# Kernel optimization log

Hardware: AMD Instinct MI355X
Metric: run time of the kernel (lower is better)

Reference implementation:

```python
import jax, jax.numpy as jnp
import numpy as np
from jax import lax

VOCAB, EMB, HID, MAXD, NCLS = 50000, 512, 512, 1024, 20
S, B = 512, 64

def setup_inputs() -> dict:
    key = jax.random.key(0)
    ks = jax.random.split(key, 16)
    sc = 0.05
    return {
        "inp": jax.random.randint(ks[0], (S, B), 0, VOCAB),
        "emb_table": jax.random.normal(ks[1], (VOCAB, EMB), jnp.float32) * sc,
        "c_l0": jax.random.normal(ks[2], (HID,), jnp.float32) * sc,
        "c_r0": jax.random.normal(ks[3], (HID,), jnp.float32) * sc,
        "W_l": jax.random.normal(ks[4], (HID, HID), jnp.float32) * sc,
        "b_l": jnp.zeros((HID,), jnp.float32),
        "W_r": jax.random.normal(ks[5], (HID, HID), jnp.float32) * sc,
        "b_r": jnp.zeros((HID,), jnp.float32),
        "W_sl": jax.random.normal(ks[6], (HID, EMB), jnp.float32) * sc,
        "b_sl": jnp.zeros((HID,), jnp.float32),
        "W_sr": jax.random.normal(ks[7], (EMB, HID), jnp.float32) * sc,  # emb_dim==hid_dim required by source
        "b_sr": jnp.zeros((EMB,), jnp.float32),
        "W_max": jax.random.normal(ks[8], (MAXD, 2 * HID + EMB), jnp.float32) * sc,
        "b_max": jnp.zeros((MAXD,), jnp.float32),
        "W_doc": jax.random.normal(ks[9], (NCLS, MAXD), jnp.float32) * sc,
        "b_doc": jnp.zeros((NCLS,), jnp.float32),
    }

def reference(inp, emb_table, c_l0, c_r0, W_l, b_l, W_r, b_r,
              W_sl, b_sl, W_sr, b_sr, W_max, b_max, W_doc, b_doc):
    # inp: [S, B] int; emb: [S, B, E]
    emb = emb_table[inp]
    # precomputed per-token projections (done once, outside the recurrence)
    emb_ls = jnp.einsum('sbe,he->sbh', emb, W_sl) + b_sl  # [S,B,H]
    emb_rs = jnp.einsum('sbe,he->sbh', emb, W_sr) + b_sr  # [S,B,H]

    def step(W, b):
        def f(c, e):  # c: [B,H], e: [B,H]
            c = jnp.tanh(c @ W.T + b + e)
            return c, c
        return f

    batch = inp.shape[1]
    c_l_init = jnp.broadcast_to(c_l0, (batch, HID))
    c_r_init = jnp.broadcast_to(c_r0, (batch, HID))
    _, c_ls = lax.scan(step(W_l, b_l), c_l_init, emb_ls)          # [S,B,H] left-to-right
    _, c_rs_rev = lax.scan(step(W_r, b_r), c_r_init, emb_rs[::-1])  # scanned right-to-left
    c_rs = c_rs_rev[::-1]                                          # re-aligned to positions

    cat = jnp.concatenate([c_ls, emb, c_rs], axis=2)               # [S,B,2H+E]
    y = jnp.tanh(jnp.einsum('sbc,mc->sbm', cat, W_max) + b_max)    # [S,B,M]
    y_max = jnp.max(y, axis=0)                                     # [B,M] max-pool over seq
    logits = y_max @ W_doc.T + b_doc                               # [B,C]
    return jax.nn.log_softmax(logits, axis=-1)
```

## Files before the change

kernel.cpp:

```cpp
#include <hip/hip_runtime.h>
#include <hip/hip_bf16.h>
#include <cstdint>
#include <cstddef>

#define SS   512
#define BB   64
#define EMBD 512
#define HIDD 512
#define MAXD 1024
#define NCLS 20
#define KCAT 1536
#define ROWS (SS*BB)

__device__ __forceinline__ uint16_t f2bf(float f) {
  uint32_t u = __float_as_uint(f);
  uint32_t r = u + 0x7fffu + ((u >> 16) & 1u);
  return (uint16_t)(r >> 16);
}
__device__ __forceinline__ float bf2f(uint32_t h) {
  return __uint_as_float(h << 16);
}
__device__ __forceinline__ uint32_t pk2(float a, float b) {
  return (uint32_t)f2bf(a) | ((uint32_t)f2bf(b) << 16);
}

__device__ __forceinline__ float fast_tanh(float x) {
  float ax = __builtin_fabsf(x);
  float e  = __builtin_amdgcn_exp2f(ax * -2.885390081777927f);
  float r  = (1.f - e) * __builtin_amdgcn_rcpf(1.f + e);
  return __builtin_copysignf(r, x);
}

#if defined(__has_builtin)
#if __has_builtin(__builtin_amdgcn_fdot2_f32_bf16)
#define USE_BF16_DOT2 1
#endif
#endif

#ifdef USE_BF16_DOT2
typedef __bf16 bf16x2_t __attribute__((ext_vector_type(2)));
__device__ __forceinline__ float dot2bf(uint32_t w, uint32_t c, float acc) {
  return __builtin_amdgcn_fdot2_f32_bf16(__builtin_bit_cast(bf16x2_t, w),
                                         __builtin_bit_cast(bf16x2_t, c), acc, false);
}
#else
__device__ __forceinline__ float dot2bf(uint32_t w, uint32_t c, float acc) {
  float w0 = __uint_as_float(w << 16);
  float w1 = __uint_as_float(w & 0xffff0000u);
  float c0 = __uint_as_float(c << 16);
  float c1 = __uint_as_float(c & 0xffff0000u);
  return fmaf(w1, c1, fmaf(w0, c0, acc));
}
#endif

__device__ __forceinline__ void gl_lds16(const void* g, void* l) {
  __builtin_amdgcn_global_load_lds((const __attribute__((address_space(1))) void*)g,
                                   (__attribute__((address_space(3))) void*)l,
                                   16, 0, 0);
}

typedef short v8s __attribute__((ext_vector_type(8)));
typedef float v4f __attribute__((ext_vector_type(4)));

__global__ __launch_bounds__(256) void prep_kernel(
    const int* __restrict__ inp, const float* __restrict__ table,
    const float* __restrict__ Wsl, const float* __restrict__ Wsr,
    const float* __restrict__ Wl,  const float* __restrict__ Wr,
    const float* __restrict__ Wmax,
    uint16_t* __restrict__ cat, uint16_t* __restrict__ wslb,
    uint16_t* __restrict__ wsrb, uint16_t* __restrict__ wlb,
    uint16_t* __restrict__ wrb, uint16_t* __restrict__ wmaxb)
{
  const int blk = blockIdx.x, t = threadIdx.x;
  if (blk < 8192) {
    const int r = blk * 4 + (t >> 6);
    const int lane = t & 63;
    const int token = inp[r];
    const float4* src = (const float4*)(table + (size_t)token * EMBD);
    uint16_t* dst = cat + (size_t)r * KCAT + 512;
#pragma unroll
    for (int p = 0; p < 2; ++p) {
      const int slot = lane + 64 * p;
      float4 v = src[slot];
      uint2 o;
      o.x = pk2(v.x, v.y);
      o.y = pk2(v.z, v.w);
      *(uint2*)(dst + slot * 4) = o;
    }
  } else {
    size_t flat = (size_t)(blk - 8192) * 2048 + (size_t)t * 8;
    const float* src; uint16_t* dst; size_t off;
    if (flat < 262144)       { src = Wsl;  dst = wslb;  off = flat; }
    else if (flat < 524288)  { src = Wsr;  dst = wsrb;  off = flat - 262144; }
    else if (flat < 786432)  { src = Wl;   dst = wlb;   off = flat - 524288; }
    else if (flat < 1048576) { src = Wr;   dst = wrb;   off = flat - 786432; }
    else                     { src = Wmax; dst = wmaxb; off = flat - 1048576; }
    float4 v0 = *(const float4*)(src + off);
    float4 v1 = *(const float4*)(src + off + 4);
    uint4 o;
    o.x = pk2(v0.x, v0.y); o.y = pk2(v0.z, v0.w);
    o.z = pk2(v1.x, v1.y); o.w = pk2(v1.z, v1.w);
    *(uint4*)(dst + off) = o;
  }
}

template<int MODE>
__global__ __launch_bounds__(256, 2) void gemm_kernel(
    const uint16_t* __restrict__ A, int lda, int K,
    const uint16_t* __restrict__ W0, const uint16_t* __restrict__ W1,
    const float* __restrict__ bias0, const float* __restrict__ bias1,
    uint16_t* __restrict__ outb, float* __restrict__ partial)
{
  __shared__ unsigned char smem[32768];
  uint16_t* lA = (uint16_t*)smem;
  uint16_t* lW = (uint16_t*)(smem + 16384);

  const int tid = threadIdx.x;
  const int mb = blockIdx.x, nb = blockIdx.y;
  const int m0 = mb * 128, n0 = nb * 128;

  const uint16_t* Wp = W0;
  const float* biasp = bias0;
  int nr0 = n0;
  if (MODE == 0 && n0 >= 512) { Wp = W1; biasp = bias1; nr0 = n0 - 512; }

  const int w = tid >> 6, lane = tid & 63;
  const int mw = w & 1, nw = w >> 1;

  v4f acc[4][4];
#pragma unroll
  for (int i = 0; i < 4; ++i)
#pragma unroll
    for (int j = 0; j < 4; ++j) {
      v4f z = {0.f, 0.f, 0.f, 0.f};
      acc[i][j] = z;
    }

  const int r_st = tid >> 3;
  const int u_st = tid & 7;

  for (int kk = 0; kk < K; kk += 64) {
    __syncthreads();
#pragma unroll
    for (int p = 0; p < 4; ++p) {
      const int r = p * 32 + r_st;
      gl_lds16(A + (size_t)(m0 + r) * lda + kk + u_st * 8, lA + (p * 256 + tid) * 8);
    }
#pragma unroll
    for (int p = 0; p < 4; ++p) {
      const int r = p * 32 + r_st;
      gl_lds16(Wp + (size_t)(nr0 + r) * K + kk + u_st * 8, lW + (p * 256 + tid) * 8);
    }
    __syncthreads();
#pragma unroll
    for (int ks = 0; ks < 2; ++ks) {
      v8s af[4], wf[4];
#pragma unroll
      for (int i = 0; i < 4; ++i)
        af[i] = *(const v8s*)&lA[(mw * 64 + i * 16 + (lane & 15)) * 64 + ks * 32 + (lane >> 4) * 8];
#pragma unroll
      for (int j = 0; j < 4; ++j)
        wf[j] = *(const v8s*)&lW[(nw * 64 + j * 16 + (lane & 15)) * 64 + ks * 32 + (lane >> 4) * 8];
#pragma unroll
      for (int i = 0; i < 4; ++i)
#pragma unroll
        for (int j = 0; j < 4; ++j)
          acc[i][j] = __builtin_amdgcn_mfma_f32_16x16x32_bf16(af[i], wf[j], acc[i][j], 0, 0, 0);
    }
  }

  __syncthreads();

  if (MODE == 0) {
#pragma unroll
    for (int i = 0; i < 4; ++i)
#pragma unroll
      for (int j = 0; j < 4; ++j) {
        const int nl = nw * 64 + j * 16 + (lane & 15);
        const float bv = biasp[nr0 + nl];
        const int colg = n0 + nl;
#pragma unroll
        for (int r = 0; r < 4; ++r) {
          const int rowg = m0 + mw * 64 + i * 16 + (lane >> 4) * 4 + r;
          outb[(size_t)rowg * 1024 + colg] = f2bf(acc[i][j][r] + bv);
        }
      }
  } else {
    float* lred = (float*)smem;
    if (mw == 1) {
#pragma unroll
      for (int i = 0; i < 4; ++i)
#pragma unroll
        for (int j = 0; j < 4; ++j) {
          const int nl = nw * 64 + j * 16 + (lane & 15);
          const float bv = biasp[nr0 + nl];
#pragma unroll
          for (int r = 0; r < 4; ++r) {
            const int bl = i * 16 + (lane >> 4) * 4 + r;
            lred[bl * 128 + nl] = fast_tanh(acc[i][j][r] + bv);
          }
        }
    }
    __syncthreads();
    if (mw == 0) {
#pragma unroll
      for (int i = 0; i < 4; ++i)
#pragma unroll
        for (int j = 0; j < 4; ++j) {
          const int nl = nw * 64 + j * 16 + (lane & 15);
          const float bv = biasp[nr0 + nl];
#pragma unroll
          for (int r = 0; r < 4; ++r) {
            const int bl = i * 16 + (lane >> 4) * 4 + r;
            const float v = fast_tanh(acc[i][j][r] + bv);
            partial[((size_t)mb * 64 + bl) * 1024 + n0 + nl] = fmaxf(v, lred[bl * 128 + nl]);
          }
        }
    }
  }
}

__global__ __launch_bounds__(512, 1) void scan_kernel(
    const uint16_t* __restrict__ ee,
    const uint16_t* __restrict__ wlb, const uint16_t* __restrict__ wrb,
    const float* __restrict__ bl, const float* __restrict__ br,
    const float* __restrict__ cl0, const float* __restrict__ cr0,
    uint16_t* __restrict__ cat,
    uint64_t* __restrict__ cbuf)
{
  const int tid = threadIdx.x;
  const int bid = blockIdx.x;
  const int b    = bid & 63;
  const int d    = (bid >> 6) & 1;
  const int half = bid >> 7;
  const int lane = tid & 63;

  const int hp = tid & 127;
  const int kq = tid >> 7;
  const bool remote = (kq >> 1) != half;

  __shared__ __align__(16) uint32_t cfull[256];
  __shared__ float2 part2[4 * 128];

  uint32_t wAa[64], wBa[64];
  {
    const uint16_t* wsrc = (d ? wrb : wlb) + (size_t)(half * 256 + 2 * hp) * HIDD + kq * 128;
    const uint4* pA = (const uint4*)wsrc;
    const uint4* pB = (const uint4*)(wsrc + HIDD);
#pragma unroll
    for (int j = 0; j < 16; ++j) {
      uint4 qa = pA[j], qb = pB[j];
      wAa[4 * j] = qa.x; wAa[4 * j + 1] = qa.y; wAa[4 * j + 2] = qa.z; wAa[4 * j + 3] = qa.w;
      wBa[4 * j] = qb.x; wBa[4 * j + 1] = qb.y; wBa[4 * j + 2] = qb.z; wBa[4 * j + 3] = qb.w;
    }
  }
  if (tid < 256) {
    const float* c0v = d ? cr0 : cl0;
    float2 cv0 = ((const float2*)c0v)[tid];
    cfull[tid] = pk2(cv0.x, cv0.y);
  }

  const int fbase = half * 256;
  const unsigned ft = (unsigned)(tid - fbase);
  const int fp = tid - fbase;

  float2 biasv = {0.f, 0.f};
  if (ft < 128u) {
    const float* bvec = d ? br : bl;
    biasv = ((const float2*)bvec)[half * 128 + fp];
  }
  __syncthreads();

  const size_t ecol = (size_t)(d * 512 + half * 256 + 2 * fp);
  const int fcol = (d ? 1024 : 0) + half * 256 + 2 * fp;

  const int pslot = ((kq & 1) << 6) | lane;
  const int pbid  = bid ^ 128;

  uint32_t ep0 = 0, ep1 = 0;
  if (ft < 128u) {
    const int s0i = d ? 511 : 0;
    const int s1i = d ? 510 : 1;
    ep0 = *(const uint32_t*)&ee[(size_t)(s0i * BB + b) * 1024 + ecol];
    ep1 = *(const uint32_t*)&ee[(size_t)(s1i * BB + b) * 1024 + ecol];
  }

  uint32_t prPrev = 0;
  int sPrev = -1;

  for (int i = 0; i < 512; ++i) {
    const int s = d ? (511 - i) : i;
    uint32_t ep2 = 0;
    if (ft < 128u) {
      const int i2 = (i + 2) & 511;
      const int s2 = d ? (511 - i2) : i2;
      ep2 = *(const uint32_t*)&ee[(size_t)(s2 * BB + b) * 1024 + ecol];
      if (sPrev >= 0)
        *(uint32_t*)&cat[(size_t)(sPrev * BB + b) * KCAT + fcol] = prPrev;
    }

    uint32_t cv;
    if (remote && i != 0) {
      const uint64_t want = (uint64_t)(uint32_t)i;
      const uint64_t* slot = &cbuf[(size_t)(((((i & 1) ^ 1)) * 256 + pbid) * 128 + pslot)];
      uint64_t v = __hip_atomic_load(slot, __ATOMIC_RELAXED, __HIP_MEMORY_SCOPE_AGENT);
      while ((v >> 32) != want) {
        __builtin_amdgcn_s_sleep(1);
        v = __hip_atomic_load(slot, __ATOMIC_RELAXED, __HIP_MEMORY_SCOPE_AGENT);
      }
      cv = (uint32_t)v;
    } else {
      cv = cfull[kq * 64 + lane];
    }

    {
      float a0 = 0.f, a1 = 0.f, a2 = 0.f, a3 = 0.f;
#pragma unroll
      for (int j = 0; j < 32; ++j) {
        const uint32_t cj0 = __builtin_amdgcn_readlane(cv, 2 * j);
        const uint32_t cj1 = __builtin_amdgcn_readlane(cv, 2 * j + 1);
        a0 = dot2bf(wAa[2 * j],     cj0, a0);
        a2 = dot2bf(wBa[2 * j],     cj0, a2);
        a1 = dot2bf(wAa[2 * j + 1], cj1, a1);
        a3 = dot2bf(wBa[2 * j + 1], cj1, a3);
      }
      float2 pv; pv.x = a0 + a1; pv.y = a2 + a3;
      part2[kq * 128 + hp] = pv;
    }

    __syncthreads();

    if (ft < 128u) {
      float2 q0 = part2[fp];
      float2 q1 = part2[128 + fp];
      float2 q2 = part2[256 + fp];
      float2 q3 = part2[384 + fp];
      float s0 = ((q0.x + q1.x) + (q2.x + q3.x)) + biasv.x + bf2f(ep0 & 0xffffu);
      float s1 = ((q0.y + q1.y) + (q2.y + q3.y)) + biasv.y + bf2f(ep0 >> 16);
      uint32_t pr = pk2(fast_tanh(s0), fast_tanh(s1));
      if (i != 511) {
        uint64_t pkt = ((uint64_t)(uint32_t)(i + 1) << 32) | (uint64_t)pr;
        __hip_atomic_store(&cbuf[(size_t)(((i & 1) * 256 + bid) * 128 + fp)],
                           pkt, __ATOMIC_RELAXED, __HIP_MEMORY_SCOPE_AGENT);
        cfull[half * 128 + fp] = pr;
        prPrev = pr; sPrev = s;
      } else {
        *(uint32_t*)&cat[(size_t)(s * BB + b) * KCAT + fcol] = pr;
      }
    }

    if (i == 511) break;
    __syncthreads();

    ep0 = ep1; ep1 = ep2;
  }
}

__global__ __launch_bounds__(256) void final_kernel(
    const float* __restrict__ partial, const float* __restrict__ Wdoc,
    const float* __restrict__ bdoc, float* __restrict__ out)
{
  const int b = blockIdx.x, t = threadIdx.x;
  __shared__ float ym[1024];
  __shared__ float lg[32];
  float m0 = -2.f, m1 = -2.f, m2 = -2.f, m3 = -2.f;
  for (int mg = 0; mg < 256; ++mg) {
    const float* p = partial + ((size_t)mg * 64 + b) * 1024;
    m0 = fmaxf(m0, p[t]);
    m1 = fmaxf(m1, p[t + 256]);
    m2 = fmaxf(m2, p[t + 512]);
    m3 = fmaxf(m3, p[t + 768]);
  }
  ym[t] = m0; ym[t + 256] = m1; ym[t + 512] = m2; ym[t + 768] = m3;
  __syncthreads();
  if (t < NCLS) {
    const float* wr = Wdoc + (size_t)t * 1024;
    float a0 = 0.f, a1 = 0.f, a2 = 0.f, a3 = 0.f;
    for (int n = 0; n < 1024; n += 4) {
      a0 = fmaf(ym[n], wr[n], a0);
      a1 = fmaf(ym[n + 1], wr[n + 1], a1);
      a2 = fmaf(ym[n + 2], wr[n + 2], a2);
      a3 = fmaf(ym[n + 3], wr[n + 3], a3);
    }
    lg[t] = (a0 + a1) + (a2 + a3) + bdoc[t];
  }
  __syncthreads();
  if (t < NCLS) {
    float mx = -1e30f;
    for (int c = 0; c < NCLS; ++c) mx = fmaxf(mx, lg[c]);
    float ssum = 0.f;
    for (int c = 0; c < NCLS; ++c) ssum += expf(lg[c] - mx);
    out[b * NCLS + t] = lg[t] - mx - logf(ssum);
  }
}

extern "C" void kernel_launch(void* const* d_in, const int* in_sizes, int n_in,
                              void* d_out, int out_size, void* d_ws, size_t ws_size,
                              hipStream_t stream) {
  const int*   inp   = (const int*)  d_in[0];
  const float* table = (const float*)d_in[1];
  const float* cl0   = (const float*)d_in[2];
  const float* cr0   = (const float*)d_in[3];
  const float* Wl    = (const float*)d_in[4];
  const float* bl    = (const float*)d_in[5];
  const float* Wr    = (const float*)d_in[6];
  const float* br    = (const float*)d_in[7];
  const float* Wsl   = (const float*)d_in[8];
  const float* bsl   = (const float*)d_in[9];
  const float* Wsr   = (const float*)d_in[10];
  const float* bsr   = (const float*)d_in[11];
  const float* Wmax  = (const float*)d_in[12];
  const float* bmax  = (const float*)d_in[13];
  const float* Wdoc  = (const float*)d_in[14];
  const float* bdoc  = (const float*)d_in[15];

  uint8_t* ws = (uint8_t*)d_ws;
  uint16_t* cat     = (uint16_t*)(ws);
  uint16_t* ee      = (uint16_t*)(ws + 100663296);
  float*    partial = (float*)   (ws + 167772160);
  uint16_t* wslb    = (uint16_t*)(ws + 234881024);
  uint16_t* wsrb    = (uint16_t*)(ws + 235405312);
  uint16_t* wmaxb   = (uint16_t*)(ws + 235929600);
  uint16_t* wlb     = (uint16_t*)(ws + 239075328);
  uint16_t* wrb     = (uint16_t*)(ws + 239599616);
  uint64_t* cbuf    = (uint64_t*)(ws + 167772160);

  prep_kernel<<<9472, 256, 0, stream>>>(inp, table, Wsl, Wsr, Wl, Wr, Wmax,
                                        cat, wslb, wsrb, wlb, wrb, wmaxb);
  gemm_kernel<0><<<dim3(256, 8), 256, 0, stream>>>(cat + 512, KCAT, 512, wslb, wsrb,
                                                   bsl, bsr, ee, nullptr);
  scan_kernel<<<256, 512, 0, stream>>>(ee, wlb, wrb, bl, br, cl0, cr0, cat, cbuf);
  gemm_kernel<1><<<dim3(256, 8), 256, 0, stream>>>(cat, KCAT, KCAT, wmaxb, nullptr,
                                                   bmax, nullptr, nullptr, partial);
  final_kernel<<<64, 256, 0, stream>>>(partial, Wdoc, bdoc, (float*)d_out);
}
```

Before: 1.028 ms.

## Batch scan recurrence over 16 sequences per block using MFMA bf16

```diff
diff --git a/kernel.cpp b/kernel.cpp
--- a/kernel.cpp
+++ b/kernel.cpp
@@ -30,28 +30,6 @@
   float r  = (1.f - e) * __builtin_amdgcn_rcpf(1.f + e);
   return __builtin_copysignf(r, x);
 }
-
-#if defined(__has_builtin)
-#if __has_builtin(__builtin_amdgcn_fdot2_f32_bf16)
-#define USE_BF16_DOT2 1
-#endif
-#endif
-
-#ifdef USE_BF16_DOT2
-typedef __bf16 bf16x2_t __attribute__((ext_vector_type(2)));
-__device__ __forceinline__ float dot2bf(uint32_t w, uint32_t c, float acc) {
-  return __builtin_amdgcn_fdot2_f32_bf16(__builtin_bit_cast(bf16x2_t, w),
-                                         __builtin_bit_cast(bf16x2_t, c), acc, false);
-}
-#else
-__device__ __forceinline__ float dot2bf(uint32_t w, uint32_t c, float acc) {
-  float w0 = __uint_as_float(w << 16);
-  float w1 = __uint_as_float(w & 0xffff0000u);
-  float c0 = __uint_as_float(c << 16);
-  float c1 = __uint_as_float(c & 0xffff0000u);
-  return fmaf(w1, c1, fmaf(w0, c0, acc));
-}
-#endif
 
 __device__ __forceinline__ void gl_lds16(const void* g, void* l) {
   __builtin_amdgcn_global_load_lds((const __attribute__((address_space(1))) void*)g,
@@ -230,130 +208,161 @@
 {
   const int tid = threadIdx.x;
   const int bid = blockIdx.x;
-  const int b    = bid & 63;
-  const int d    = (bid >> 6) & 1;
-  const int half = bid >> 7;
+  const int half = bid >> 3;
+  const int g    = (bid >> 1) & 3;
+  const int d    = bid & 1;
+  const int bg   = g * 16;
+  const int pbid = bid ^ 8;
+
+  const int w    = tid >> 6;
   const int lane = tid & 63;
-
-  const int hp = tid & 127;
-  const int kq = tid >> 7;
-  const bool remote = (kq >> 1) != half;
-
-  __shared__ __align__(16) uint32_t cfull[256];
-  __shared__ float2 part2[4 * 128];
-
-  uint32_t wAa[64], wBa[64];
+  const int m4   = (lane >> 4) * 4;
+  const int ncol = lane & 15;
+  const int h0   = half * 256 + w * 32 + ncol;
+  const int h1   = h0 + 16;
+  const int ph0  = (1 - half) * 256 + w * 32 + ncol;
+  const int ph1  = ph0 + 16;
+
+  __shared__ __align__(16) uint16_t Abuf[2][8192];
+
+#define SWZ(batch, chunk) ((((batch) * 64) + ((chunk) ^ ((batch) & 7))) * 16)
+
+  const uint16_t* wsrc = d ? wrb : wlb;
+
+  v8s wf0[16], wf1[16];
   {
-    const uint16_t* wsrc = (d ? wrb : wlb) + (size_t)(half * 256 + 2 * hp) * HIDD + kq * 128;
-    const uint4* pA = (const uint4*)wsrc;
-    const uint4* pB = (const uint4*)(wsrc + HIDD);
-#pragma unroll
-    for (int j = 0; j < 16; ++j) {
-      uint4 qa = pA[j], qb = pB[j];
-      wAa[4 * j] = qa.x; wAa[4 * j + 1] = qa.y; wAa[4 * j + 2] = qa.z; wAa[4 * j + 3] = qa.w;
-      wBa[4 * j] = qb.x; wBa[4 * j + 1] = qb.y; wBa[4 * j + 2] = qb.z; wBa[4 * j + 3] = qb.w;
-    }
-  }
-  if (tid < 256) {
+    const uint16_t* p0 = wsrc + (size_t)h0 * 512 + (lane >> 4) * 8;
+    const uint16_t* p1 = wsrc + (size_t)h1 * 512 + (lane >> 4) * 8;
+#pragma unroll
+    for (int kt = 0; kt < 16; ++kt) {
+      wf0[kt] = *(const v8s*)(p0 + kt * 32);
+      wf1[kt] = *(const v8s*)(p1 + kt * 32);
+    }
+  }
+
+  {
     const float* c0v = d ? cr0 : cl0;
-    float2 cv0 = ((const float2*)c0v)[tid];
-    cfull[tid] = pk2(cv0.x, cv0.y);
-  }
-
-  const int fbase = half * 256;
-  const unsigned ft = (unsigned)(tid - fbase);
-  const int fp = tid - fbase;
-
-  float2 biasv = {0.f, 0.f};
-  if (ft < 128u) {
-    const float* bvec = d ? br : bl;
-    biasv = ((const float2*)bvec)[half * 128 + fp];
-  }
+    const int batch = tid >> 5;
+#pragma unroll
+    for (int cc = 0; cc < 2; ++cc) {
+      const int chunk = (tid & 31) * 2 + cc;
+      const float* src = c0v + chunk * 8;
+      uint4 o;
+      o.x = pk2(src[0], src[1]); o.y = pk2(src[2], src[3]);
+      o.z = pk2(src[4], src[5]); o.w = pk2(src[6], src[7]);
+      *(uint4*)((char*)Abuf[0] + SWZ(batch, chunk)) = o;
+    }
+  }
+
+  const float* bvec = d ? br : bl;
+  const float bias0v = bvec[h0];
+  const float bias1v = bvec[h1];
+
+  const int ec0 = d * 512 + h0, ec1 = d * 512 + h1;
+  uint32_t erA[8], erB[8];
+  {
+    const int s0 = d ? 511 : 0, s1 = d ? 510 : 1;
+#pragma unroll
+    for (int r = 0; r < 4; ++r) {
+      erA[r]     = *(const uint16_t*)&ee[(size_t)(s0 * 64 + bg + m4 + r) * 1024 + ec0];
+      erA[4 + r] = *(const uint16_t*)&ee[(size_t)(s0 * 64 + bg + m4 + r) * 1024 + ec1];
+      erB[r]     = *(const uint16_t*)&ee[(size_t)(s1 * 64 + bg + m4 + r) * 1024 + ec0];
+      erB[4 + r] = *(const uint16_t*)&ee[(size_t)(s1 * 64 + bg + m4 + r) * 1024 + ec1];
+    }
+  }
+
+  const int catbase = (d ? 1024 : 0) + half * 256;
+  const int rbBatch = tid >> 5, rbCl = tid & 31;
+  const int rbChunk = half * 32 + rbCl;
+
   __syncthreads();
 
-  const size_t ecol = (size_t)(d * 512 + half * 256 + 2 * fp);
-  const int fcol = (d ? 1024 : 0) + half * 256 + 2 * fp;
-
-  const int pslot = ((kq & 1) << 6) | lane;
-  const int pbid  = bid ^ 128;
-
-  uint32_t ep0 = 0, ep1 = 0;
-  if (ft < 128u) {
-    const int s0i = d ? 511 : 0;
-    const int s1i = d ? 510 : 1;
-    ep0 = *(const uint32_t*)&ee[(size_t)(s0i * BB + b) * 1024 + ecol];
-    ep1 = *(const uint32_t*)&ee[(size_t)(s1i * BB + b) * 1024 + ecol];
-  }
-
-  uint32_t prPrev = 0;
-  int sPrev = -1;
-
-  for (int i = 0; i < 512; ++i) {
-    const int s = d ? (511 - i) : i;
-    uint32_t ep2 = 0;
-    if (ft < 128u) {
-      const int i2 = (i + 2) & 511;
-      const int s2 = d ? (511 - i2) : i2;
-      ep2 = *(const uint32_t*)&ee[(size_t)(s2 * BB + b) * 1024 + ecol];
-      if (sPrev >= 0)
-        *(uint32_t*)&cat[(size_t)(sPrev * BB + b) * KCAT + fcol] = prPrev;
-    }
-
-    uint32_t cv;
-    if (remote && i != 0) {
-      const uint64_t want = (uint64_t)(uint32_t)i;
-      const uint64_t* slot = &cbuf[(size_t)(((((i & 1) ^ 1)) * 256 + pbid) * 128 + pslot)];
-      uint64_t v = __hip_atomic_load(slot, __ATOMIC_RELAXED, __HIP_MEMORY_SCOPE_AGENT);
-      while ((v >> 32) != want) {
-        __builtin_amdgcn_s_sleep(1);
-        v = __hip_atomic_load(slot, __ATOMIC_RELAXED, __HIP_MEMORY_SCOPE_AGENT);
-      }
-      cv = (uint32_t)v;
+  auto step = [&](int i, uint32_t (&er)[8]) {
+    if (i > 0) {
+      const int sP = d ? (512 - i) : (i - 1);
+      uint4 v = *(const uint4*)((char*)Abuf[i & 1] + SWZ(rbBatch, rbChunk));
+      *(uint4*)&cat[(size_t)(sP * 64 + bg + rbBatch) * KCAT + catbase + rbCl * 8] = v;
+    }
+
+    v4f a00 = {0.f, 0.f, 0.f, 0.f}, a01 = {0.f, 0.f, 0.f, 0.f};
+    v4f a10 = {0.f, 0.f, 0.f, 0.f}, a11 = {0.f, 0.f, 0.f, 0.f};
+#pragma unroll
+    for (int kt = 0; kt < 16; ++kt) {
+      v8s af = *(const v8s*)((char*)Abuf[i & 1] + SWZ(lane & 15, kt * 4 + (lane >> 4)));
+      if (kt & 1) {
+        a01 = __builtin_amdgcn_mfma_f32_16x16x32_bf16(af, wf0[kt], a01, 0, 0, 0);
+        a11 = __builtin_amdgcn_mfma_f32_16x16x32_bf16(af, wf1[kt], a11, 0, 0, 0);
+      } else {
+        a00 = __builtin_amdgcn_mfma_f32_16x16x32_bf16(af, wf0[kt], a00, 0, 0, 0);
+        a10 = __builtin_amdgcn_mfma_f32_16x16x32_bf16(af, wf1[kt], a10, 0, 0, 0);
+      }
+    }
+
+    float v0[4], v1[4];
+#pragma unroll
+    for (int r = 0; r < 4; ++r) {
+      v0[r] = fast_tanh(a00[r] + a01[r] + bias0v + bf2f(er[r]));
+      v1[r] = fast_tanh(a10[r] + a11[r] + bias1v + bf2f(er[4 + r]));
+    }
+
+    if (i < 510) {
+      const int s2 = d ? (509 - i) : (i + 2);
+#pragma unroll
+      for (int r = 0; r < 4; ++r) {
+        er[r]     = *(const uint16_t*)&ee[(size_t)(s2 * 64 + bg + m4 + r) * 1024 + ec0];
+        er[4 + r] = *(const uint16_t*)&ee[(size_t)(s2 * 64 + bg + m4 + r) * 1024 + ec1];
+      }
+    }
+
+    char* An = (char*)Abuf[(i + 1) & 1];
+    if (i != 511) {
+      const uint64_t want = (uint64_t)(uint32_t)(i + 1);
+#pragma unroll
+      for (int r = 0; r < 4; ++r) {
+        uint64_t pkt = (want << 32) | (uint64_t)pk2(v0[r], v1[r]);
+        __hip_atomic_store(&cbuf[(size_t)(((i & 1) * 16 + bid) * 2048 + tid * 4 + r)],
+                           pkt, __ATOMIC_RELAXED, __HIP_MEMORY_SCOPE_AGENT);
+      }
+#pragma unroll
+      for (int r = 0; r < 4; ++r) {
+        *(uint16_t*)(An + SWZ(m4 + r, h0 >> 3) + (h0 & 7) * 2) = f2bf(v0[r]);
+        *(uint16_t*)(An + SWZ(m4 + r, h1 >> 3) + (h1 & 7) * 2) = f2bf(v1[r]);
+      }
+      __builtin_amdgcn_sched_barrier(0);
+#pragma unroll
+      for (int r = 0; r < 4; ++r) {
+        const uint64_t* slot =
+            &cbuf[(size_t)(((i & 1) * 16 + pbid) * 2048 + tid * 4 + r)];
+        uint64_t v = __hip_atomic_load(slot, __ATOMIC_RELAXED, __HIP_MEMORY_SCOPE_AGENT);
+        while ((v >> 32) != want) {
+          __builtin_amdgcn_s_sleep(1);
+          v = __hip_atomic_load(slot, __ATOMIC_RELAXED, __HIP_MEMORY_SCOPE_AGENT);
+        }
+        *(uint16_t*)(An + SWZ(m4 + r, ph0 >> 3) + (ph0 & 7) * 2) = (uint16_t)(v & 0xffffu);
+        *(uint16_t*)(An + SWZ(m4 + r, ph1 >> 3) + (ph1 & 7) * 2) = (uint16_t)((v >> 16) & 0xffffu);
+      }
+      __syncthreads();
     } else {
-      cv = cfull[kq * 64 + lane];
-    }
-
-    {
-      float a0 = 0.f, a1 = 0.f, a2 = 0.f, a3 = 0.f;
-#pragma unroll
-      for (int j = 0; j < 32; ++j) {
-        const uint32_t cj0 = __builtin_amdgcn_readlane(cv, 2 * j);
-        const uint32_t cj1 = __builtin_amdgcn_readlane(cv, 2 * j + 1);
-        a0 = dot2bf(wAa[2 * j],     cj0, a0);
-        a2 = dot2bf(wBa[2 * j],     cj0, a2);
-        a1 = dot2bf(wAa[2 * j + 1], cj1, a1);
-        a3 = dot2bf(wBa[2 * j + 1], cj1, a3);
-      }
-      float2 pv; pv.x = a0 + a1; pv.y = a2 + a3;
-      part2[kq * 128 + hp] = pv;
-    }
-
-    __syncthreads();
-
-    if (ft < 128u) {
-      float2 q0 = part2[fp];
-      float2 q1 = part2[128 + fp];
-      float2 q2 = part2[256 + fp];
-      float2 q3 = part2[384 + fp];
-      float s0 = ((q0.x + q1.x) + (q2.x + q3.x)) + biasv.x + bf2f(ep0 & 0xffffu);
-      float s1 = ((q0.y + q1.y) + (q2.y + q3.y)) + biasv.y + bf2f(ep0 >> 16);
-      uint32_t pr = pk2(fast_tanh(s0), fast_tanh(s1));
-      if (i != 511) {
-        uint64_t pkt = ((uint64_t)(uint32_t)(i + 1) << 32) | (uint64_t)pr;
-        __hip_atomic_store(&cbuf[(size_t)(((i & 1) * 256 + bid) * 128 + fp)],
-                           pkt, __ATOMIC_RELAXED, __HIP_MEMORY_SCOPE_AGENT);
-        cfull[half * 128 + fp] = pr;
-        prPrev = pr; sPrev = s;
-      } else {
-        *(uint32_t*)&cat[(size_t)(s * BB + b) * KCAT + fcol] = pr;
-      }
-    }
-
-    if (i == 511) break;
-    __syncthreads();
-
-    ep0 = ep1; ep1 = ep2;
-  }
+#pragma unroll
+      for (int r = 0; r < 4; ++r) {
+        *(uint16_t*)(An + SWZ(m4 + r, h0 >> 3) + (h0 & 7) * 2) = f2bf(v0[r]);
+        *(uint16_t*)(An + SWZ(m4 + r, h1 >> 3) + (h1 & 7) * 2) = f2bf(v1[r]);
+      }
+    }
+  };
+
+  for (int ii = 0; ii < 256; ++ii) {
+    step(2 * ii, erA);
+    step(2 * ii + 1, erB);
+  }
+
+  __syncthreads();
+  {
+    const int sL = d ? 0 : 511;
+    uint4 v = *(const uint4*)((char*)Abuf[0] + SWZ(rbBatch, rbChunk));
+    *(uint4*)&cat[(size_t)(sL * 64 + bg + rbBatch) * KCAT + catbase + rbCl * 8] = v;
+  }
+#undef SWZ
 }
 
 __global__ __launch_bounds__(256) void final_kernel(
@@ -429,7 +438,7 @@
                                         cat, wslb, wsrb, wlb, wrb, wmaxb);
   gemm_kernel<0><<<dim3(256, 8), 256, 0, stream>>>(cat + 512, KCAT, 512, wslb, wsrb,
                                                    bsl, bsr, ee, nullptr);
-  scan_kernel<<<256, 512, 0, stream>>>(ee, wlb, wrb, bl, br, cl0, cr0, cat, cbuf);
+  scan_kernel<<<16, 512, 0, stream>>>(ee, wlb, wrb, bl, br, cl0, cr0, cat, cbuf);
   gemm_kernel<1><<<dim3(256, 8), 256, 0, stream>>>(cat, KCAT, KCAT, wmaxb, nullptr,
                                                    bmax, nullptr, nullptr, partial);
   final_kernel<<<64, 256, 0, stream>>>(partial, Wdoc, bdoc, (float*)d_out);
```

Result: slower. 1.830 ms (+78.0%).
